# Kernel optimization log

Measured on AMD Instinct MI355X. Metric: run time of the kernel, lower is better.

Reference implementation:

```python
import jax, jax.numpy as jnp
import numpy as np

DIM = 512
H = 8
HS = DIM // H
SCALES = [25, 12, 7]
ATTN_SCALE = HS ** -0.5
EPS = 1e-5


def _ln(x, g, b):
    m = jnp.mean(x, axis=-1, keepdims=True)
    v = jnp.mean((x - m) ** 2, axis=-1, keepdims=True)
    return (x - m) * jax.lax.rsqrt(v + EPS) * g + b


def setup_inputs() -> dict:
    key = jax.random.key(0)
    ks = jax.random.split(key, 12)
    B, T, J, C = 64, 64, 25, DIM
    w = lambda k, s: jax.random.normal(k, s, dtype=jnp.float32) * 0.02
    return {
        "src": jax.random.normal(ks[0], (B, T, J, C), dtype=jnp.float32),
        "spatial_relation": jax.random.normal(ks[1], (B, T, J, J, 2), dtype=jnp.float32),
        "ln1_g": jnp.ones((C,), jnp.float32),
        "ln1_b": jnp.zeros((C,), jnp.float32),
        "Wq": w(ks[2], (3, C, C)),
        "Wk": w(ks[3], (3, C, C)),
        "Wv": w(ks[4], (3, C, C)),
        "pool0_fc1_w": w(ks[5], (C, 2 * C)),
        "pool0_fc1_b": jnp.zeros((2 * C,), jnp.float32),
        "pool0_fc2_w": w(ks[6], (2 * C, SCALES[1])),
        "pool0_fc2_b": jnp.zeros((SCALES[1],), jnp.float32),
        "pool1_fc1_w": w(ks[7], (C, 2 * C)),
        "pool1_fc1_b": jnp.zeros((2 * C,), jnp.float32),
        "pool1_fc2_w": w(ks[8], (2 * C, SCALES[2])),
        "pool1_fc2_b": jnp.zeros((SCALES[2],), jnp.float32),
    }


def reference(src, spatial_relation, ln1_g, ln1_b, Wq, Wk, Wv,
              pool0_fc1_w, pool0_fc1_b, pool0_fc2_w, pool0_fc2_b,
              pool1_fc1_w, pool1_fc1_b, pool1_fc2_w, pool1_fc2_b):
    # NOTE: in the original torch module, the relation-bias terms (R_qk, R_conv,
    # attn_R_qurt) and spatial_relation_emb are computed but never added to the
    # attention logits, so they do not affect the output; faithful output math below.
    B, T, J, C = src.shape
    x = src.reshape(B * T, J, C)
    g_feat = x  # global (query) features, stay at J nodes
    l_feat = x  # local (key/value) features, get pooled
    pools = [
        (pool0_fc1_w, pool0_fc1_b, pool0_fc2_w, pool0_fc2_b),
        (pool1_fc1_w, pool1_fc1_b, pool1_fc2_w, pool1_fc2_b),
    ]
    outs = []
    for i in range(len(SCALES)):
        qn = _ln(g_feat, ln1_g, ln1_b)
        kn = _ln(l_feat, ln1_g, ln1_b)
        q = (qn @ Wq[i]).reshape(B * T, J, H, HS)
        k = (kn @ Wk[i]).reshape(B * T, -1, H, HS)
        v = (kn @ Wv[i]).reshape(B * T, -1, H, HS)
        logits = jnp.einsum('bnhd,bmhd->bhnm', q, k) * ATTN_SCALE
        a = jax.nn.softmax(logits, axis=-1)
        o = jnp.einsum('bhnm,bmhd->bnhd', a, v).reshape(B * T, J, C)
        outs.append(g_feat + o)
        if i < len(SCALES) - 1:
            f1w, f1b, f2w, f2b = pools[i]
            h = jax.nn.gelu(l_feat @ f1w + f1b, approximate=False)
            S = jax.nn.softmax(h @ f2w + f2b, axis=-1)  # (BT, Ni, Ni+1)
            l_feat = jnp.einsum('bns,bnc->bsc', S, l_feat)
    return jnp.mean(jnp.stack(outs, axis=-1), axis=-1)
```

## Files before the change

### kernel.cpp

```cpp
#include <hip/hip_runtime.h>

typedef unsigned short u16;
typedef unsigned int   u32;
typedef _Float16 f16;
typedef __attribute__((ext_vector_type(8))) unsigned short u16x8;
typedef __attribute__((ext_vector_type(8))) _Float16 f16x8;
typedef __attribute__((ext_vector_type(2))) _Float16 f16x2;
typedef __attribute__((ext_vector_type(4))) float f32x4;

__device__ __forceinline__ u16 f2h(float f) {
  f16 h = (f16)f;
  return __builtin_bit_cast(u16, h);
}
__device__ __forceinline__ float h2f(u16 u) {
  return (float)__builtin_bit_cast(f16, u);
}

__global__ __launch_bounds__(256) void prep_w(const float* __restrict__ Wq,
    const float* __restrict__ Wk, const float* __restrict__ Wv,
    const float* __restrict__ f0, const float* __restrict__ f1,
    u16* __restrict__ wt) {
  int t = blockIdx.x * 256 + threadIdx.x;
  float v;
  if (t < 786432) {
    int i = t >> 18, r = t & 262143, n = r >> 9, k = r & 511;
    v = Wq[(size_t)(i << 18) + k * 512 + n];
  } else if (t < 2359296) {
    int r = t - 786432, i = r >> 19, r2 = r & 524287;
    int n = (r2 >> 9) & 511, k = r2 & 511;
    v = ((r2 >> 18) ? Wv : Wk)[(size_t)(i << 18) + k * 512 + n];
  } else if (t < 2883584) {
    int r = t - 2359296, n = r >> 9, k = r & 511;
    v = f0[(size_t)k * 1024 + n];
  } else {
    int r = t - 2883584, n = r >> 9, k = r & 511;
    v = f1[(size_t)k * 1024 + n];
  }
  wt[t] = f2h(v);
}

__global__ __launch_bounds__(256) void ln_f32(const float* __restrict__ x,
    const float* __restrict__ g, const float* __restrict__ bta,
    u16* __restrict__ xn, u16* __restrict__ xb) {
  int row = (blockIdx.x << 2) + (threadIdx.x >> 6);
  int lane = threadIdx.x & 63;
  const float* xr = x + (size_t)row * 512 + (lane << 3);
  float4 a = *(const float4*)xr;
  float4 c = *(const float4*)(xr + 4);
  float v[8] = {a.x, a.y, a.z, a.w, c.x, c.y, c.z, c.w};
  float s = 0.f, s2 = 0.f;
#pragma unroll
  for (int j = 0; j < 8; ++j) { s += v[j]; s2 += v[j] * v[j]; }
  for (int off = 32; off; off >>= 1) { s += __shfl_xor(s, off); s2 += __shfl_xor(s2, off); }
  float mean = s * (1.f / 512.f);
  float var = s2 * (1.f / 512.f) - mean * mean;
  float rs = rsqrtf(var + 1e-5f);
  const float* gp = g + (lane << 3);
  const float* bp = bta + (lane << 3);
  u16x8 pb, pn;
#pragma unroll
  for (int j = 0; j < 8; ++j) {
    pb[j] = f2h(v[j]);
    pn[j] = f2h((v[j] - mean) * rs * gp[j] + bp[j]);
  }
  *(u16x8*)(xb + (size_t)row * 512 + (lane << 3)) = pb;
  *(u16x8*)(xn + (size_t)row * 512 + (lane << 3)) = pn;
}

__global__ __launch_bounds__(256) void ln_b16(const u16* __restrict__ xin,
    const float* __restrict__ g, const float* __restrict__ bta,
    u16* __restrict__ xout) {
  int row = (blockIdx.x << 2) + (threadIdx.x >> 6);
  int lane = threadIdx.x & 63;
  f16x8 u = *(const f16x8*)(xin + (size_t)row * 512 + (lane << 3));
  float v[8];
#pragma unroll
  for (int j = 0; j < 8; ++j) v[j] = (float)u[j];
  float s = 0.f, s2 = 0.f;
#pragma unroll
  for (int j = 0; j < 8; ++j) { s += v[j]; s2 += v[j] * v[j]; }
  for (int off = 32; off; off >>= 1) { s += __shfl_xor(s, off); s2 += __shfl_xor(s2, off); }
  float mean = s * (1.f / 512.f);
  float var = s2 * (1.f / 512.f) - mean * mean;
  float rs = rsqrtf(var + 1e-5f);
  const float* gp = g + (lane << 3);
  const float* bp = bta + (lane << 3);
  u16x8 pn;
#pragma unroll
  for (int j = 0; j < 8; ++j) pn[j] = f2h((v[j] - mean) * rs * gp[j] + bp[j]);
  *(u16x8*)(xout + (size_t)row * 512 + (lane << 3)) = pn;
}

template <bool GELU>
__global__ __launch_bounds__(256, 4) void gemm_bt(const u16* __restrict__ A,
    const u16* __restrict__ Bt, u16* __restrict__ C,
    const float* __restrict__ bias, int M, int N) {
  __shared__ __align__(16) char smem[34816];
  u16* Cs = (u16*)smem;
  constexpr int LDC = 136;
  int tid = threadIdx.x;
  int w = tid >> 6, lane = tid & 63;
  int nwg = gridDim.x * gridDim.y;
  int wg = blockIdx.x + gridDim.x * blockIdx.y;
  int swz = (wg & 7) * (nwg >> 3) + (wg >> 3);
  int m0 = (swz / gridDim.x) << 7, n0 = (swz % gridDim.x) << 7;
  int wm = (w & 1) << 6, wn = (w >> 1) << 6;
  f32x4 acc[4][4] = {};
  const int grow = tid >> 3;
  const int gcol = (((tid & 7) ^ (grow & 7)) << 3);
  for (int kt = 0; kt < 8; ++kt) {
    __syncthreads();
    {
      u16* dA = (u16*)smem;
      u16* dB = (u16*)(smem + 16384);
#pragma unroll
      for (int s = 0; s < 4; ++s) {
        const u16* gA = A + (size_t)(m0 + grow + (s << 5)) * 512 + (kt << 6) + gcol;
        __builtin_amdgcn_global_load_lds(
            (const __attribute__((address_space(1))) u32*)gA,
            (__attribute__((address_space(3))) u32*)(dA + tid * 8 + (s << 11)), 16, 0, 0);
      }
#pragma unroll
      for (int s = 0; s < 4; ++s) {
        const u16* gB = Bt + (size_t)(n0 + grow + (s << 5)) * 512 + (kt << 6) + gcol;
        __builtin_amdgcn_global_load_lds(
            (const __attribute__((address_space(1))) u32*)gB,
            (__attribute__((address_space(3))) u32*)(dB + tid * 8 + (s << 11)), 16, 0, 0);
      }
    }
    asm volatile("s_waitcnt vmcnt(0)" ::: "memory");
    __syncthreads();
    const u16* As = (const u16*)smem;
    const u16* Bs = (const u16*)(smem + 16384);
#pragma unroll
    for (int kk = 0; kk < 2; ++kk) {
      int slot_w = (kk << 2) + (lane >> 4);
      f16x8 af[4], bfr[4];
#pragma unroll
      for (int mi = 0; mi < 4; ++mi) {
        int rr = wm + (mi << 4) + (lane & 15);
        af[mi] = *(const f16x8*)(As + rr * 64 + ((slot_w ^ (rr & 7)) << 3));
      }
#pragma unroll
      for (int ni = 0; ni < 4; ++ni) {
        int rr = wn + (ni << 4) + (lane & 15);
        bfr[ni] = *(const f16x8*)(Bs + rr * 64 + ((slot_w ^ (rr & 7)) << 3));
      }
#pragma unroll
      for (int mi = 0; mi < 4; ++mi)
#pragma unroll
        for (int ni = 0; ni < 4; ++ni)
          acc[mi][ni] = __builtin_amdgcn_mfma_f32_16x16x32_f16(af[mi], bfr[ni], acc[mi][ni], 0, 0, 0);
    }
  }
  __syncthreads();
  int cr = (lane >> 4) << 2, cc = lane & 15;
#pragma unroll
  for (int mi = 0; mi < 4; ++mi) {
#pragma unroll
    for (int ni = 0; ni < 4; ++ni) {
      float bv = 0.f;
      if (GELU) bv = bias[n0 + wn + (ni << 4) + cc];
#pragma unroll
      for (int j = 0; j < 4; ++j) {
        float v = acc[mi][ni][j];
        if (GELU) { v += bv; v = 0.5f * v * (1.f + erff(v * 0.70710678118f)); }
        Cs[(wm + (mi << 4) + cr + j) * LDC + wn + (ni << 4) + cc] = f2h(v);
      }
    }
  }
  __syncthreads();
  int r = tid >> 1, hc = (tid & 1) << 6;
  u16* crow = C + (size_t)(m0 + r) * N + n0 + hc;
  const u16* srow = Cs + r * LDC + hc;
#pragma unroll
  for (int i = 0; i < 8; ++i)
    *(u16x8*)(crow + (i << 3)) = *(const u16x8*)(srow + (i << 3));
}

template <int NKV, int PMODE, int MINW, int G, bool DBUF>
__global__ __launch_bounds__(512, MINW) void attn(const u16* __restrict__ Q,
    const u16* __restrict__ KV, const u16* __restrict__ xb,
    float* __restrict__ out, u16* __restrict__ p) {
  constexpr int ELEMS = NKV * 1024;
  __shared__ __align__(16) u16 KVl[(DBUF ? 2 : 1)][ELEMS];
  int tid = threadIdx.x;
  int b0 = blockIdx.x * G;
  int h = tid >> 6, r = tid & 63, n = r >> 1, half = r & 1;
  int dbase = (h << 6) + (half << 5);
  bool act = (n < 25);
  f16x8 q8[4];
  if constexpr (DBUF) {
    if (act) {
      const u16* qr = Q + (size_t)(b0 * 25 + n) * 512 + dbase;
#pragma unroll
      for (int i = 0; i < 4; ++i) q8[i] = *(const f16x8*)(qr + (i << 3));
    }
    __builtin_amdgcn_sched_barrier(0);
    const u16* src = KV + (size_t)b0 * ELEMS;
    for (int e = tid * 8; e < ELEMS; e += 4096)
      __builtin_amdgcn_global_load_lds(
          (const __attribute__((address_space(1))) u32*)(src + e),
          (__attribute__((address_space(3))) u32*)(KVl[0] + e), 16, 0, 0);
    asm volatile("s_waitcnt vmcnt(0)" ::: "memory");
    __syncthreads();
  }
  for (int t = 0; t < G; ++t) {
    const u16* KVc = KVl[DBUF ? (t & 1) : 0];
    int b = b0 + t;
    size_t rowoff = (size_t)(b * 25 + n) * 512 + dbase;
    f16x8 pv16[4];
    f16x8 xv16[4];
    float4 ov[8];
    if (act) {
      if (PMODE == 3 || PMODE == 4) {
        const u16* prow = p + rowoff;
#pragma unroll
        for (int i = 0; i < 4; ++i) pv16[i] = *(const f16x8*)(prow + (i << 3));
      }
      if (PMODE == 0 || PMODE == 4) {
        const u16* xrow = xb + rowoff;
#pragma unroll
        for (int i = 0; i < 4; ++i) xv16[i] = *(const f16x8*)(xrow + (i << 3));
      }
      if (PMODE == 1) {
        const float* orow = out + rowoff;
#pragma unroll
        for (int i = 0; i < 8; ++i) ov[i] = *(const float4*)(orow + (i << 2));
      }
    }
    f16x8 qn[4];
    if constexpr (DBUF) {
      if (act && t + 1 < G) {
        const u16* qr = Q + (size_t)((b + 1) * 25 + n) * 512 + dbase;
#pragma unroll
        for (int i = 0; i < 4; ++i) qn[i] = *(const f16x8*)(qr + (i << 3));
      }
      __builtin_amdgcn_sched_barrier(0);
      if (t + 1 < G) {
        const u16* src = KV + (size_t)(b + 1) * ELEMS;
        u16* dst = KVl[(t + 1) & 1];
        for (int e = tid * 8; e < ELEMS; e += 4096)
          __builtin_amdgcn_global_load_lds(
              (const __attribute__((address_space(1))) u32*)(src + e),
              (__attribute__((address_space(3))) u32*)(dst + e), 16, 0, 0);
      }
    } else {
      if (act) {
        const u16* qr = Q + (size_t)(b * 25 + n) * 512 + dbase;
#pragma unroll
        for (int i = 0; i < 4; ++i) q8[i] = *(const f16x8*)(qr + (i << 3));
      }
      const u16* src = KV + (size_t)b * ELEMS;
      for (int e = tid * 8; e < ELEMS; e += 4096)
        __builtin_amdgcn_global_load_lds(
            (const __attribute__((address_space(1))) u32*)(src + e),
            (__attribute__((address_space(3))) u32*)(KVl[0] + e), 16, 0, 0);
      asm volatile("s_waitcnt vmcnt(0)" ::: "memory");
      __syncthreads();
    }
    if (act) {
      const f16x2* q2 = (const f16x2*)q8;
      float s[NKV];
      float mx = -1e30f;
#pragma unroll
      for (int m = 0; m < NKV; ++m) {
        const u16* kr = KVc + m * 1024 + dbase;
        f16x2 a0 = {(f16)0.f, (f16)0.f}, a1 = a0;
#pragma unroll
        for (int i = 0; i < 4; ++i) {
          f16x8 kv = *(const f16x8*)(kr + (i << 3));
          const f16x2* k2 = (const f16x2*)&kv;
          a0 += q2[i * 4 + 0] * k2[0];
          a1 += q2[i * 4 + 1] * k2[1];
          a0 += q2[i * 4 + 2] * k2[2];
          a1 += q2[i * 4 + 3] * k2[3];
        }
        f16x2 at = a0 + a1;
        float d = (float)at[0] + (float)at[1];
        d += __shfl_xor(d, 1);
        s[m] = d * 0.125f;
        mx = fmaxf(mx, s[m]);
      }
      float sum = 0.f;
#pragma unroll
      for (int m = 0; m < NKV; ++m) { s[m] = __expf(s[m] - mx); sum += s[m]; }
      f16x8 o8[4] = {};
#pragma unroll
      for (int m = 0; m < NKV; ++m) {
        f16 ah = (f16)s[m];
        f16x8 av = {ah, ah, ah, ah, ah, ah, ah, ah};
        const u16* vr = KVc + m * 1024 + 512 + dbase;
#pragma unroll
        for (int i = 0; i < 4; ++i) {
          f16x8 vv = *(const f16x8*)(vr + (i << 3));
          o8[i] += vv * av;
        }
      }
      if (PMODE == 0 || PMODE == 1) {
        float sc = (1.f / sum) * (1.f / 3.f);
        float* orow = out + rowoff;
#pragma unroll
        for (int i = 0; i < 4; ++i) {
#pragma unroll
          for (int j = 0; j < 8; j += 4) {
            float4 rr;
            if (PMODE == 0) {
              rr.x = (float)o8[i][j + 0] * sc + (float)xv16[i][j + 0];
              rr.y = (float)o8[i][j + 1] * sc + (float)xv16[i][j + 1];
              rr.z = (float)o8[i][j + 2] * sc + (float)xv16[i][j + 2];
              rr.w = (float)o8[i][j + 3] * sc + (float)xv16[i][j + 3];
            } else {
              float4 pv = ov[i * 2 + (j >> 2)];
              rr.x = (float)o8[i][j + 0] * sc + pv.x;
              rr.y = (float)o8[i][j + 1] * sc + pv.y;
              rr.z = (float)o8[i][j + 2] * sc + pv.z;
              rr.w = (float)o8[i][j + 3] * sc + pv.w;
            }
            *(float4*)(orow + (i << 3) + j) = rr;
          }
        }
      } else if (PMODE == 2 || PMODE == 3) {
        float sc = 1.f / sum;
        u16* prow = p + rowoff;
#pragma unroll
        for (int i = 0; i < 4; ++i) {
          u16x8 pk;
#pragma unroll
          for (int j = 0; j < 8; ++j) {
            float v = (float)o8[i][j] * sc;
            if (PMODE == 3) v += (float)pv16[i][j];
            pk[j] = f2h(v);
          }
          *(u16x8*)(prow + (i << 3)) = pk;
        }
      } else {
        float sc = 1.f / sum;
        float* orow = out + rowoff;
#pragma unroll
        for (int i = 0; i < 4; ++i) {
#pragma unroll
          for (int j = 0; j < 8; j += 4) {
            float4 rr;
            rr.x = (float)xv16[i][j + 0] + ((float)pv16[i][j + 0] + (float)o8[i][j + 0] * sc) * (1.f / 3.f);
            rr.y = (float)xv16[i][j + 1] + ((float)pv16[i][j + 1] + (float)o8[i][j + 1] * sc) * (1.f / 3.f);
            rr.z = (float)xv16[i][j + 2] + ((float)pv16[i][j + 2] + (float)o8[i][j + 2] * sc) * (1.f / 3.f);
            rr.w = (float)xv16[i][j + 3] + ((float)pv16[i][j + 3] + (float)o8[i][j + 3] * sc) * (1.f / 3.f);
            *(float4*)(orow + (i << 3) + j) = rr;
          }
        }
      }
    }
    if constexpr (DBUF) {
      asm volatile("s_waitcnt vmcnt(0)" ::: "memory");
      __syncthreads();
#pragma unroll
      for (int i = 0; i < 4; ++i) q8[i] = qn[i];
    } else {
      if (t + 1 < G) __syncthreads();
    }
  }
}

template <int NIN, int NOUT>
__global__ __launch_bounds__(256) void pool(const u16* __restrict__ h,
    const u16* __restrict__ lf, const float* __restrict__ w2,
    const float* __restrict__ b2, u16* __restrict__ lout) {
  __shared__ __align__(16) float W2l[1024 * NOUT];
  __shared__ __align__(16) u16 Xl[NIN * 512];
  __shared__ __align__(16) float Sl[NIN * NOUT];
  int b = blockIdx.x, tid = threadIdx.x;
  for (int e = tid; e < 1024 * NOUT; e += 256) W2l[e] = w2[e];
  for (int e = tid * 8; e < NIN * 512; e += 2048)
    *(u16x8*)(Xl + e) = *(const u16x8*)(lf + (size_t)b * NIN * 512 + e);
  __syncthreads();
  if (tid < NIN * 8) {
    int nn = tid >> 3, sub = tid & 7;
    float pl[NOUT] = {};
    const u16* hr = h + (size_t)(b * NIN + nn) * 1024;
    for (int cc = 0; cc < 128; ++cc) {
      int c = sub + (cc << 3);
      float hv = h2f(hr[c]);
#pragma unroll
      for (int s2 = 0; s2 < NOUT; ++s2) pl[s2] += hv * W2l[c * NOUT + s2];
    }
#pragma unroll
    for (int s2 = 0; s2 < NOUT; ++s2) {
      pl[s2] += __shfl_down(pl[s2], 4, 8);
      pl[s2] += __shfl_down(pl[s2], 2, 8);
      pl[s2] += __shfl_down(pl[s2], 1, 8);
    }
    if (sub == 0) {
      float mx = -1e30f;
#pragma unroll
      for (int s2 = 0; s2 < NOUT; ++s2) { pl[s2] += b2[s2]; mx = fmaxf(mx, pl[s2]); }
      float sum = 0.f;
#pragma unroll
      for (int s2 = 0; s2 < NOUT; ++s2) { pl[s2] = __expf(pl[s2] - mx); sum += pl[s2]; }
      float inv = 1.f / sum;
#pragma unroll
      for (int s2 = 0; s2 < NOUT; ++s2) Sl[nn * NOUT + s2] = pl[s2] * inv;
    }
  }
  __syncthreads();
  int c0 = tid << 1;
#pragma unroll
  for (int s2 = 0; s2 < NOUT; ++s2) {
    float a0 = 0.f, a1 = 0.f;
#pragma unroll
    for (int nn = 0; nn < NIN; ++nn) {
      float wv = Sl[nn * NOUT + s2];
      a0 += wv * h2f(Xl[nn * 512 + c0]);
      a1 += wv * h2f(Xl[nn * 512 + c0 + 1]);
    }
    u32 pk = (u32)f2h(a0) | ((u32)f2h(a1) << 16);
    *(u32*)(lout + (size_t)(b * NOUT + s2) * 512 + c0) = pk;
  }
}

extern "C" void kernel_launch(void* const* d_in, const int* in_sizes, int n_in,
                              void* d_out, int out_size, void* d_ws, size_t ws_size,
                              hipStream_t stream) {
  const float* src = (const float*)d_in[0];
  const float* g    = (const float*)d_in[2];
  const float* bt   = (const float*)d_in[3];
  const float* Wq   = (const float*)d_in[4];
  const float* Wk   = (const float*)d_in[5];
  const float* Wv   = (const float*)d_in[6];
  const float* f0w  = (const float*)d_in[7];
  const float* f0b  = (const float*)d_in[8];
  const float* f0w2 = (const float*)d_in[9];
  const float* f0b2 = (const float*)d_in[10];
  const float* f1w  = (const float*)d_in[11];
  const float* f1b  = (const float*)d_in[12];
  const float* f1w2 = (const float*)d_in[13];
  const float* f1b2 = (const float*)d_in[14];
  float* out = (float*)d_out;
  char* ws = (char*)d_ws;

  u16* wt  = (u16*)(ws + 0);
  u16* xn  = (u16*)(ws + 6815744);
  u16* xb  = (u16*)(ws + 111673344);
  u16* qb  = (u16*)(ws + 216530944);
  u16* B1  = (u16*)(ws + 321388544);
  u16* l1  = (u16*)(ws + 426246144);
  u16* kn1 = (u16*)(ws + 476577792);
  u16* l2  = qb;
  u16* kn2 = qb + 14680064;
  bool bigws = ws_size >= 640000000ull;
  u16* pbuf = (u16*)(ws + 526909440);

  prep_w<<<13312, 256, 0, stream>>>(Wq, Wk, Wv, f0w, f1w, wt);
  ln_f32<<<25600, 256, 0, stream>>>(src, g, bt, xn, xb);

  gemm_bt<false><<<dim3(4, 800), 256, 0, stream>>>(xn, wt, qb, nullptr, 102400, 512);
  for (int s = 0; s < 2; ++s) {
    size_t ro = (size_t)s * 51200;
    gemm_bt<false><<<dim3(8, 400), 256, 0, stream>>>(xn + ro * 512, wt + 786432, B1, nullptr, 51200, 1024);
    if (bigws)
      attn<25, 2, 3, 2, false><<<1024, 512, 0, stream>>>(qb + ro * 512, B1, xb + ro * 512, out + ro * 512, pbuf + ro * 512);
    else
      attn<25, 0, 3, 2, false><<<1024, 512, 0, stream>>>(qb + ro * 512, B1, xb + ro * 512, out + ro * 512, pbuf);
  }

  for (int s = 0; s < 2; ++s) {
    size_t ro = (size_t)s * 51200;
    gemm_bt<true><<<dim3(8, 400), 256, 0, stream>>>(xb + ro * 512, wt + 2359296, B1, f0b, 51200, 1024);
    pool<25, 12><<<2048, 256, 0, stream>>>(B1, xb + ro * 512, f0w2, f0b2, l1 + (size_t)s * 2048 * 12 * 512);
  }
  ln_b16<<<12288, 256, 0, stream>>>(l1, g, bt, kn1);

  gemm_bt<false><<<dim3(4, 800), 256, 0, stream>>>(xn, wt + 262144, qb, nullptr, 102400, 512);
  gemm_bt<false><<<dim3(8, 384), 256, 0, stream>>>(kn1, wt + 786432 + 524288, B1, nullptr, 49152, 1024);
  if (bigws)
    attn<12, 3, 3, 4, true><<<1024, 512, 0, stream>>>(qb, B1, xb, out, pbuf);
  else
    attn<12, 1, 3, 4, true><<<1024, 512, 0, stream>>>(qb, B1, xb, out, pbuf);

  gemm_bt<true><<<dim3(8, 384), 256, 0, stream>>>(l1, wt + 2883584, B1, f1b, 49152, 1024);
  pool<12, 7><<<4096, 256, 0, stream>>>(B1, l1, f1w2, f1b2, l2);
  ln_b16<<<7168, 256, 0, stream>>>(l2, g, bt, kn2);

  gemm_bt<false><<<dim3(8, 224), 256, 0, stream>>>(kn2, wt + 786432 + 1048576, B1, nullptr, 28672, 1024);
  gemm_bt<false><<<dim3(4, 800), 256, 0, stream>>>(xn, wt + 524288, qb, nullptr, 102400, 512);
  if (bigws)
    attn<7, 4, 3, 4, true><<<1024, 512, 0, stream>>>(qb, B1, xb, out, pbuf);
  else
    attn<7, 1, 3, 4, true><<<1024, 512, 0, stream>>>(qb, B1, xb, out, pbuf);
}
```

Measured before the change: 1.556 ms.

## Double-buffer GEMM K-tiles with async LDS loads overlapping MFMA compute

The projection GEMM now splits K into 16 tiles of 32 instead of 8 tiles of 64 and keeps two LDS buffers. It issues the global-to-LDS load for the next tile before computing on the current one, waiting only on the older loads. This is meant to hide global memory latency behind the MFMA work. In exchange there is one more barrier per iteration, twice as many iterations, and a new XOR swizzle for the narrower tile.

Result: slower. 1.610 ms (+3.5%).

```diff
diff --git a/kernel.cpp b/kernel.cpp
--- a/kernel.cpp
+++ b/kernel.cpp
@@ -106,45 +106,52 @@
   int m0 = (swz / gridDim.x) << 7, n0 = (swz % gridDim.x) << 7;
   int wm = (w & 1) << 6, wn = (w >> 1) << 6;
   f32x4 acc[4][4] = {};
-  const int grow = tid >> 3;
-  const int gcol = (((tid & 7) ^ (grow & 7)) << 3);
-  for (int kt = 0; kt < 8; ++kt) {
+  const int grow2 = tid >> 2;
+  const int gcol = (((tid & 3) ^ ((grow2 >> 1) & 3)) << 3);
+#define GSTAGE(kt, bi)                                                          \
+  {                                                                             \
+    u16* dA = (u16*)(smem + ((bi) << 13));                                      \
+    u16* dB = (u16*)(smem + 16384 + ((bi) << 13));                              \
+    _Pragma("unroll")                                                           \
+    for (int s = 0; s < 2; ++s) {                                               \
+      const u16* gA = A + (size_t)(m0 + grow2 + (s << 6)) * 512 + ((kt) << 5) + gcol; \
+      __builtin_amdgcn_global_load_lds(                                         \
+          (const __attribute__((address_space(1))) u32*)gA,                     \
+          (__attribute__((address_space(3))) u32*)(dA + tid * 8 + (s << 11)), 16, 0, 0); \
+    }                                                                           \
+    _Pragma("unroll")                                                           \
+    for (int s = 0; s < 2; ++s) {                                               \
+      const u16* gB = Bt + (size_t)(n0 + grow2 + (s << 6)) * 512 + ((kt) << 5) + gcol; \
+      __builtin_amdgcn_global_load_lds(                                         \
+          (const __attribute__((address_space(1))) u32*)gB,                     \
+          (__attribute__((address_space(3))) u32*)(dB + tid * 8 + (s << 11)), 16, 0, 0); \
+    }                                                                           \
+  }
+  GSTAGE(0, 0);
+  const int sw_lane = ((lane & 15) >> 1) & 3;
+  for (int kt = 0; kt < 16; ++kt) {
+    if (kt + 1 < 16) {
+      GSTAGE(kt + 1, (kt + 1) & 1);
+      asm volatile("s_waitcnt vmcnt(4)" ::: "memory");
+    } else {
+      asm volatile("s_waitcnt vmcnt(0)" ::: "memory");
+    }
     __syncthreads();
+    const u16* As = (const u16*)(smem + ((kt & 1) << 13));
+    const u16* Bs = (const u16*)(smem + 16384 + ((kt & 1) << 13));
     {
-      u16* dA = (u16*)smem;
-      u16* dB = (u16*)(smem + 16384);
-#pragma unroll
-      for (int s = 0; s < 4; ++s) {
-        const u16* gA = A + (size_t)(m0 + grow + (s << 5)) * 512 + (kt << 6) + gcol;
-        __builtin_amdgcn_global_load_lds(
-            (const __attribute__((address_space(1))) u32*)gA,
-            (__attribute__((address_space(3))) u32*)(dA + tid * 8 + (s << 11)), 16, 0, 0);
-      }
-#pragma unroll
-      for (int s = 0; s < 4; ++s) {
-        const u16* gB = Bt + (size_t)(n0 + grow + (s << 5)) * 512 + (kt << 6) + gcol;
-        __builtin_amdgcn_global_load_lds(
-            (const __attribute__((address_space(1))) u32*)gB,
-            (__attribute__((address_space(3))) u32*)(dB + tid * 8 + (s << 11)), 16, 0, 0);
-      }
-    }
-    asm volatile("s_waitcnt vmcnt(0)" ::: "memory");
-    __syncthreads();
-    const u16* As = (const u16*)smem;
-    const u16* Bs = (const u16*)(smem + 16384);
-#pragma unroll
-    for (int kk = 0; kk < 2; ++kk) {
-      int slot_w = (kk << 2) + (lane >> 4);
+      int slot_w = lane >> 4;
+      int sl = (slot_w ^ sw_lane) << 3;
       f16x8 af[4], bfr[4];
 #pragma unroll
       for (int mi = 0; mi < 4; ++mi) {
         int rr = wm + (mi << 4) + (lane & 15);
-        af[mi] = *(const f16x8*)(As + rr * 64 + ((slot_w ^ (rr & 7)) << 3));
+        af[mi] = *(const f16x8*)(As + (rr << 5) + sl);
       }
 #pragma unroll
       for (int ni = 0; ni < 4; ++ni) {
         int rr = wn + (ni << 4) + (lane & 15);
-        bfr[ni] = *(const f16x8*)(Bs + rr * 64 + ((slot_w ^ (rr & 7)) << 3));
+        bfr[ni] = *(const f16x8*)(Bs + (rr << 5) + sl);
       }
 #pragma unroll
       for (int mi = 0; mi < 4; ++mi)
@@ -152,8 +159,9 @@
         for (int ni = 0; ni < 4; ++ni)
           acc[mi][ni] = __builtin_amdgcn_mfma_f32_16x16x32_f16(af[mi], bfr[ni], acc[mi][ni], 0, 0, 0);
     }
-  }
-  __syncthreads();
+    __syncthreads();
+  }
+#undef GSTAGE
   int cr = (lane >> 4) << 2, cc = lane & 15;
 #pragma unroll
   for (int mi = 0; mi < 4; ++mi) {
```
